# Performance work log

Measured on AMD Instinct MI355X. Metric: run time of the kernel, lower is better.

Reference implementation:

```python
import jax, jax.numpy as jnp
import numpy as np

DIM = 1024
HEADS = 16
HEAD_DIM = DIM // HEADS


def rotate_half(x):
    x1, x2 = jnp.split(x, 2, axis=-1)
    return jnp.concatenate((-x2, x1), axis=-1)


def rope_tables(T, D, dtype=jnp.float32):
    inv_freq = 1.0 / (10000.0 ** (jnp.arange(0, D, 2, dtype=jnp.float32) / D))
    t = jnp.arange(T, dtype=jnp.float32)
    freqs = jnp.einsum('i,j->ij', t, inv_freq)  # [T, D/2]
    emb = jnp.concatenate((freqs, freqs), axis=-1)  # [T, D]
    return emb.astype(dtype), jnp.cos(emb).astype(dtype), jnp.sin(emb).astype(dtype)


def setup_inputs() -> dict:
    key = jax.random.key(0)
    kx, kq, kk, kv, ko = jax.random.split(key, 5)
    B, T = 2, 4096
    scale = 1.0 / np.sqrt(DIM)
    x = jax.random.normal(kx, (B, T, DIM), dtype=jnp.float32)
    wq = jax.random.normal(kq, (DIM, DIM), dtype=jnp.float32) * scale
    wk = jax.random.normal(kk, (DIM, DIM), dtype=jnp.float32) * scale
    wv = jax.random.normal(kv, (DIM, DIM), dtype=jnp.float32) * scale
    wo = jax.random.normal(ko, (DIM, DIM), dtype=jnp.float32) * scale
    return {"x": x, "wq": wq, "wk": wk, "wv": wv, "wo": wo}


def reference(x, wq, wk, wv, wo):
    B, T, C = x.shape
    H, D = HEADS, HEAD_DIM
    # projections; nn.Linear applies x @ W^T
    q = (x @ wq.T).reshape(B, T, H, D).transpose(0, 2, 1, 3)  # [B,H,T,D]
    k = (x @ wk.T).reshape(B, T, H, D).transpose(0, 2, 1, 3)
    v = (x @ wv.T).reshape(B, T, H, D).transpose(0, 2, 1, 3)
    _, cos, sin = rope_tables(T, D, x.dtype)
    cos = cos[None, None]  # [1,1,T,D]
    sin = sin[None, None]
    q = q * cos + rotate_half(q) * sin
    k = k * cos + rotate_half(k) * sin
    scores = jnp.einsum('bhtd,bhsd->bhts', q, k) / jnp.sqrt(jnp.asarray(D, x.dtype))
    attn = jax.nn.softmax(scores, axis=-1)
    out = jnp.einsum('bhts,bhsd->bhtd', attn, v)
    out = out.transpose(0, 2, 1, 3).reshape(B, T, C)
    return out @ wo.T
```

## Files before the change

### kernel.cpp

```cpp
#include <hip/hip_runtime.h>
#include <hip/hip_bf16.h>
#include <math.h>


typedef __attribute__((ext_vector_type(8))) short short8;
typedef __attribute__((ext_vector_type(4))) short short4v;
typedef __attribute__((ext_vector_type(4))) float floatx4;

using bf16 = __hip_bfloat16;

static constexpr int T_ = 4096;
static constexpr int C_ = 1024;
static constexpr int M_ = 8192;
static constexpr float QSCALE = 0.125f * 1.44269504088896340736f;

#if __has_builtin(__builtin_amdgcn_mfma_f32_16x16x16bf16_1k)
#define USE_K16 1
#else
#define USE_K16 0
#endif

#if __has_builtin(__builtin_amdgcn_exp2f)
#define EXP2 __builtin_amdgcn_exp2f
#else
#define EXP2 exp2f
#endif

__device__ __forceinline__ floatx4 mfma16(short8 a, short8 b, floatx4 c) {
    return __builtin_amdgcn_mfma_f32_16x16x32_bf16(a, b, c, 0, 0, 0);
}
#if USE_K16
__device__ __forceinline__ floatx4 mfma_k16(short4v a, short4v b, floatx4 c) {
    return __builtin_amdgcn_mfma_f32_16x16x16bf16_1k(a, b, c, 0, 0, 0);
}
#endif

__device__ __forceinline__ short8 ld8(const bf16* p) {
    return *reinterpret_cast<const short8*>(p);
}
__device__ __forceinline__ short4v ld4(const bf16* p) {
    return *reinterpret_cast<const short4v*>(p);
}
__device__ __forceinline__ void st8(bf16* p, short8 v) {
    *reinterpret_cast<short8*>(p) = v;
}
__device__ __forceinline__ unsigned short f2bf(float x) {
    bf16 h = __float2bfloat16(x);
    return reinterpret_cast<unsigned short&>(h);
}

__device__ __forceinline__ int pack2bf(float a, float b, unsigned sel) {
    const unsigned ua = __float_as_uint(a) + 0x8000u;
    const unsigned ub = __float_as_uint(b) + 0x8000u;
    int r;
    asm("v_perm_b32 %0, %1, %2, %3" : "=v"(r) : "v"(ub), "v"(ua), "s"(sel));
    return r;
}
__device__ __forceinline__ short4v i2s4(int lo, int hi) {
    union { int2 i; short4v s; } u;
    u.i.x = lo; u.i.y = hi;
    return u.s;
}
__device__ __forceinline__ short8 i2s8(int a, int b, int c, int d) {
    union { int4 i; short8 s; } u;
    u.i.x = a; u.i.y = b; u.i.z = c; u.i.w = d;
    return u.s;
}

__device__ __forceinline__ void cp16(const bf16* g, bf16* l) {
    __builtin_amdgcn_global_load_lds(
        (const __attribute__((address_space(1))) void*)g,
        (__attribute__((address_space(3))) void*)l, 16, 0, 0);
}

__global__ __launch_bounds__(256)
void prep_kernel(const float* __restrict__ x,
                 const float* __restrict__ wq, const float* __restrict__ wk,
                 const float* __restrict__ wv, const float* __restrict__ wo,
                 bf16* __restrict__ xb, bf16* __restrict__ wqb,
                 float2* __restrict__ CS) {
    const int blk = blockIdx.x;
    if (blk < 6144) {
        const float* in;
        bf16* out;
        int i;
        if (blk < 4096) {
            i = blk * 256 + threadIdx.x;
            in = x; out = xb;
        } else {
            i = (blk - 4096) * 256 + threadIdx.x;
            const int seg = i >> 17;
            const int off = i & 131071;
            in = (seg == 0) ? wq : (seg == 1) ? wk : (seg == 2) ? wv : wo;
            out = wqb + (size_t)i * 8 - (size_t)off * 8;
            i = off;
        }
        const float4* p = reinterpret_cast<const float4*>(in) + (size_t)i * 2;
        const float4 a = p[0];
        const float4 b = p[1];
        short8 v;
        v[0] = (short)f2bf(a.x); v[1] = (short)f2bf(a.y);
        v[2] = (short)f2bf(a.z); v[3] = (short)f2bf(a.w);
        v[4] = (short)f2bf(b.x); v[5] = (short)f2bf(b.y);
        v[6] = (short)f2bf(b.z); v[7] = (short)f2bf(b.w);
        *(reinterpret_cast<short8*>(out) + i) = v;
    } else {
        const int i = (blk - 6144) * 256 + threadIdx.x;
        const int t = i >> 5;
        const int j = i & 31;
        const float inv_freq = expf(-(float)j * 0.28782313662425575f);
        float s, c;
        sincosf((float)t * inv_freq, &s, &c);
        CS[i] = make_float2(c, s);
    }
}

#define GEMM_PROLOGUE(Ab, Wb)                                                 \
    _Pragma("unroll")                                                         \
    for (int j = 0; j < 2; ++j) {                                             \
        const int row = srow + j * 64;                                        \
        cp16((Ab) + (size_t)row * C_ + scol, &Als[0][(j * 256 + tid) * 8]);   \
        cp16((Wb) + (size_t)row * C_ + scol, &Bls[0][(j * 256 + tid) * 8]);   \
    }                                                                         \
    _Pragma("unroll")                                                         \
    for (int j = 0; j < 2; ++j) {                                             \
        const int row = srow + j * 64;                                        \
        cp16((Ab) + (size_t)row * C_ + 32 + scol, &Als[1][(j * 256 + tid) * 8]); \
        cp16((Wb) + (size_t)row * C_ + 32 + scol, &Bls[1][(j * 256 + tid) * 8]); \
    }

#define KSTEP(Ab, Wb, KK, BUF, LB, DOISSUE, VMN)                              \
    do {                                                                      \
        asm volatile("s_waitcnt vmcnt(" VMN ")" ::: "memory");                \
        __builtin_amdgcn_sched_barrier(0);                                    \
        __builtin_amdgcn_s_barrier();                                         \
        __builtin_amdgcn_sched_barrier(0);                                    \
        if (DOISSUE) {                                                        \
            _Pragma("unroll")                                                 \
            for (int j = 0; j < 2; ++j) {                                     \
                const int row = srow + j * 64;                                \
                cp16((Ab) + (size_t)row * C_ + (KK) + 64 + scol,              \
                     &Als[LB][(j * 256 + tid) * 8]);                          \
                cp16((Wb) + (size_t)row * C_ + (KK) + 64 + scol,              \
                     &Bls[LB][(j * 256 + tid) * 8]);                          \
            }                                                                 \
        }                                                                     \
        short8 a[4], b[4];                                                    \
        _Pragma("unroll")                                                     \
        for (int i = 0; i < 4; ++i)                                           \
            a[i] = ld8(&Als[BUF][(wr + i * 16 + lr) * 32 + quad * 8]);        \
        _Pragma("unroll")                                                     \
        for (int j = 0; j < 4; ++j)                                           \
            b[j] = ld8(&Bls[BUF][(wc + j * 16 + lr) * 32 + quad * 8]);        \
        _Pragma("unroll")                                                     \
        for (int i = 0; i < 4; ++i)                                           \
            _Pragma("unroll")                                                 \
            for (int j = 0; j < 4; ++j)                                       \
                acc[i][j] = mfma16(a[i], b[j], acc[i][j]);                    \
    } while (0)

#define GEMM_MAINLOOP(Ab, Wb)                                                 \
    GEMM_PROLOGUE(Ab, Wb)                                                     \
    for (int kk = 0; kk < 960; kk += 96) {                                    \
        KSTEP(Ab, Wb, kk,      0, 2, 1, "4");                                 \
        KSTEP(Ab, Wb, kk + 32, 1, 0, 1, "4");                                 \
        KSTEP(Ab, Wb, kk + 64, 2, 1, 1, "4");                                 \
    }                                                                         \
    KSTEP(Ab, Wb, 960, 0, 2, 0, "4");                                         \
    KSTEP(Ab, Wb, 992, 1, 0, 0, "0");

__global__ __launch_bounds__(256)
void gemm128_kernel(const bf16* __restrict__ A, const bf16* __restrict__ W,
                    void* __restrict__ out, int mode, int ntile, int cpx) {
    const int orig = blockIdx.x;
    const int swz  = (orig & 7) * cpx + (orig >> 3);
    const int m0   = (swz / ntile) * 128;
    const int n0   = (swz % ntile) * 128;
    const int tid  = threadIdx.x;
    const int lane = tid & 63;
    const int wave = tid >> 6;
    const int quad = lane >> 4;
    const int lr   = lane & 15;
    const int wr   = (wave >> 1) * 64;
    const int wc   = (wave & 1) * 64;

    __shared__ __align__(16) bf16 Als[3][128 * 32];
    __shared__ __align__(16) bf16 Bls[3][128 * 32];

    const int srow = tid >> 2;
    const int scol = (tid & 3) * 8;

    floatx4 acc[4][4];
#pragma unroll
    for (int i = 0; i < 4; ++i)
#pragma unroll
        for (int j = 0; j < 4; ++j) acc[i][j] = floatx4{0.f, 0.f, 0.f, 0.f};

    const bf16* Ab = A + (size_t)m0 * C_;
    const bf16* Wb = W + (size_t)n0 * C_;

    GEMM_MAINLOOP(Ab, Wb)

    if (mode == 0) {
        bf16* ob = (bf16*)out;
#pragma unroll
        for (int j = 0; j < 4; ++j) {
            const int col = n0 + wc + j * 16 + lr;
#pragma unroll
            for (int i = 0; i < 4; ++i)
#pragma unroll
                for (int r = 0; r < 4; ++r) {
                    const int m = m0 + wr + i * 16 + quad * 4 + r;
                    ob[(size_t)m * C_ + col] = __float2bfloat16(acc[i][j][r]);
                }
        }
    } else {
        float* of = (float*)out;
#pragma unroll
        for (int j = 0; j < 4; ++j) {
            const int col = n0 + wc + j * 16 + lr;
#pragma unroll
            for (int i = 0; i < 4; ++i)
#pragma unroll
                for (int r = 0; r < 4; ++r) {
                    const int m = m0 + wr + i * 16 + quad * 4 + r;
                    of[(size_t)m * C_ + col] = acc[i][j][r];
                }
        }
    }
}

__global__ __launch_bounds__(256)
void gemm_qkv_kernel(const bf16* __restrict__ A, const bf16* __restrict__ W,
                     bf16* __restrict__ Qbase, const float2* __restrict__ CS) {
    const int orig = blockIdx.x;
    const int swz  = (orig & 7) * 192 + (orig >> 3);
    const int m0   = (swz / 24) * 128;
    const int n0g  = (swz % 24) * 128;
    const int tid  = threadIdx.x;
    const int lane = tid & 63;
    const int wave = tid >> 6;
    const int quad = lane >> 4;
    const int lr   = lane & 15;
    const int wr   = (wave >> 1) * 64;
    const int wc   = (wave & 1) * 64;

    __shared__ __align__(16) bf16 Als[3][128 * 32];
    __shared__ __align__(16) bf16 Bls[3][128 * 32];

    const int srow = tid >> 2;
    const int scol = (tid & 3) * 8;

    floatx4 acc[4][4];
#pragma unroll
    for (int i = 0; i < 4; ++i)
#pragma unroll
        for (int j = 0; j < 4; ++j) acc[i][j] = floatx4{0.f, 0.f, 0.f, 0.f};

    const bf16* Ab = A + (size_t)m0 * C_;
    const bf16* Wb = W + (size_t)n0g * C_;

    GEMM_MAINLOOP(Ab, Wb)

    const int seg = n0g >> 10;
    const int n0  = n0g & 1023;
    if (seg < 2) {
        bf16* ob = Qbase + (size_t)seg * M_ * C_;
        const float scale = (seg == 0) ? QSCALE : 1.0f;
        const int tb = (m0 & 4095) + wr + quad * 4;
#pragma unroll
        for (int j = 0; j < 2; ++j) {
            const int col  = n0 + wc + j * 16 + lr;
            const int jcol = j * 16 + lr;
#pragma unroll
            for (int i = 0; i < 4; ++i) {
#pragma unroll
                for (int r = 0; r < 4; ++r) {
                    const int t = tb + i * 16 + r;
                    const float2 cs = CS[t * 32 + jcol];
                    const float q1 = acc[i][j][r];
                    const float q2 = acc[i][j + 2][r];
                    const int m = m0 + wr + i * 16 + quad * 4 + r;
                    ob[(size_t)m * C_ + col] =
                        __float2bfloat16((q1 * cs.x - q2 * cs.y) * scale);
                    ob[(size_t)m * C_ + col + 32] =
                        __float2bfloat16((q2 * cs.x + q1 * cs.y) * scale);
                }
            }
        }
    } else {
        unsigned short* ob = (unsigned short*)(Qbase + (size_t)2 * M_ * C_);
        const int b2 = m0 >> 12;
#pragma unroll
        for (int j = 0; j < 4; ++j) {
            const int n = n0 + wc + j * 16 + lr;
            const int h = n >> 6;
            const int d = n & 63;
#pragma unroll
            for (int i = 0; i < 4; ++i) {
                const int t0 = (m0 & 4095) + wr + i * 16 + quad * 4;
                ushort4 v;
                v.x = f2bf(acc[i][j][0]); v.y = f2bf(acc[i][j][1]);
                v.z = f2bf(acc[i][j][2]); v.w = f2bf(acc[i][j][3]);
                size_t idx = ((size_t)((b2 * 16 + h) * 64 + d)) * T_ + t0;
                *reinterpret_cast<ushort4*>(ob + idx) = v;
            }
        }
    }
}

__global__ __launch_bounds__(256)
void attn_kernel(const bf16* __restrict__ Q, const bf16* __restrict__ K,
                 const bf16* __restrict__ Vt, bf16* __restrict__ AO) {
    const int tid  = threadIdx.x;
    const int lane = tid & 63;
    const int wave = tid >> 6;
    const int quad = lane >> 4;
    const int lr   = lane & 15;
    const int bh   = blockIdx.y;
    const int b    = bh >> 4;
    const int h    = bh & 15;
    const int q0   = blockIdx.x * 128 + wave * 32;

    const bf16* Qb = Q + (size_t)b * T_ * C_ + h * 64;
    const bf16* Kb = K + (size_t)b * T_ * C_ + h * 64;
    const bf16* Vb = Vt + (size_t)bh * 64 * T_;

#if USE_K16
    __shared__ __align__(16) bf16 Kls[2][64 * 64];
    __shared__ __align__(16) bf16 Vls[2][64 * 64];

    const int srow  = tid >> 3;
    const int sc    = tid & 7;
    const int sphys = (sc ^ (srow & 7)) * 8;
    const int soff0 = srow * 64 + sphys;
    const int soff1 = (srow + 32) * 64 + sphys;

    const unsigned psel = 0x07060302u;
    const floatx4 FZ = {0.f, 0.f, 0.f, 0.f};
    const int one2 = 0x3F803F80;
    const short8 VONE = i2s8(one2, one2, one2, one2);

    short8 aq[2][2];
#pragma unroll
    for (int t = 0; t < 2; ++t) {
        aq[t][0] = ld8(Qb + (size_t)(q0 + t * 16 + lr) * C_ + quad * 8);
        aq[t][1] = ld8(Qb + (size_t)(q0 + t * 16 + lr) * C_ + 32 + quad * 8);
    }

    floatx4 O[2][4];
#pragma unroll
    for (int t = 0; t < 2; ++t)
#pragma unroll
        for (int dt = 0; dt < 4; ++dt) O[t][dt] = floatx4{0.f, 0.f, 0.f, 0.f};
    floatx4 Osum[2] = {{0.f, 0.f, 0.f, 0.f}, {0.f, 0.f, 0.f, 0.f}};

    const int lr7    = lr & 7;
    const int kchunk = (quad ^ lr7) * 8;
    const int vsub   = (quad & 1) * 4;
    const int vbq    = quad >> 1;
    const int kel0   = lr * 64 + kchunk;
    const int kel1   = kel0 ^ 32;
    int velk[4];
#pragma unroll
    for (int kk = 0; kk < 4; ++kk)
        velk[kk] = lr * 64 + (((2 * kk + vbq) ^ lr7) * 8) + vsub;

    short8 kr0, kr1, vr0, vr1;
#define LOAD_STAGE(kv0)                                              \
    do {                                                             \
        kr0 = ld8(Kb + (size_t)((kv0) + srow) * C_ + sc * 8);        \
        kr1 = ld8(Kb + (size_t)((kv0) + srow + 32) * C_ + sc * 8);   \
        vr0 = ld8(Vb + (size_t)srow * T_ + (kv0) + sc * 8);          \
        vr1 = ld8(Vb + (size_t)(srow + 32) * T_ + (kv0) + sc * 8);   \
    } while (0)
#define STORE_STAGE(p)                                               \
    do {                                                             \
        st8(&Kls[p][soff0], kr0);                                    \
        st8(&Kls[p][soff1], kr1);                                    \
        st8(&Vls[p][soff0], vr0);                                    \
        st8(&Vls[p][soff1], vr1);                                    \
    } while (0)

#define BAR()                                                        \
    do {                                                             \
        asm volatile("s_waitcnt lgkmcnt(0)" ::: "memory");           \
        __builtin_amdgcn_s_barrier();                                \
    } while (0)

#define COMPUTE(P)                                                            \
    do {                                                                      \
        const bf16* Ks = Kls[P];                                              \
        const bf16* Vs = Vls[P];                                              \
        int prlo[2][4], prhi[2][4];                                           \
        _Pragma("unroll")                                                     \
        for (int kk = 0; kk < 4; ++kk) {                                      \
            const short8 kf0 = ld8(Ks + kk * 1024 + kel0);                    \
            const short8 kf1 = ld8(Ks + kk * 1024 + kel1);                    \
            floatx4 s0 = mfma16(kf0, aq[0][0], FZ);                           \
            s0 = mfma16(kf1, aq[0][1], s0);                                   \
            floatx4 s1 = mfma16(kf0, aq[1][0], FZ);                           \
            s1 = mfma16(kf1, aq[1][1], s1);                                   \
            const float e0 = EXP2(s0[0]), e1 = EXP2(s0[1]);                   \
            const float e2 = EXP2(s0[2]), e3 = EXP2(s0[3]);                   \
            prlo[0][kk] = pack2bf(e0, e1, psel);                              \
            prhi[0][kk] = pack2bf(e2, e3, psel);                              \
            const float f0 = EXP2(s1[0]), f1 = EXP2(s1[1]);                   \
            const float f2 = EXP2(s1[2]), f3 = EXP2(s1[3]);                   \
            prlo[1][kk] = pack2bf(f0, f1, psel);                              \
            prhi[1][kk] = pack2bf(f2, f3, psel);                              \
        }                                                                     \
        \
        Osum[0] = mfma16(i2s8(prlo[0][0], prhi[0][0], prlo[0][1], prhi[0][1]),\
                         VONE, Osum[0]);                                      \
        Osum[0] = mfma16(i2s8(prlo[0][2], prhi[0][2], prlo[0][3], prhi[0][3]),\
                         VONE, Osum[0]);                                      \
        Osum[1] = mfma16(i2s8(prlo[1][0], prhi[1][0], prlo[1][1], prhi[1][1]),\
                         VONE, Osum[1]);                                      \
        Osum[1] = mfma16(i2s8(prlo[1][2], prhi[1][2], prlo[1][3], prhi[1][3]),\
                         VONE, Osum[1]);                                      \
        __builtin_amdgcn_s_setprio(1);                                        \
        _Pragma("unroll")                                                     \
        for (int dt = 0; dt < 4; ++dt) {                                      \
            _Pragma("unroll")                                                 \
            for (int kk = 0; kk < 4; ++kk) {                                  \
                const short4v vf = ld4(Vs + dt * 1024 + velk[kk]);            \
                O[0][dt] = mfma_k16(i2s4(prlo[0][kk], prhi[0][kk]), vf, O[0][dt]); \
                O[1][dt] = mfma_k16(i2s4(prlo[1][kk], prhi[1][kk]), vf, O[1][dt]); \
            }                                                                 \
        }                                                                     \
        __builtin_amdgcn_s_setprio(0);                                        \
    } while (0)

    LOAD_STAGE(0);
    STORE_STAGE(0);
    LOAD_STAGE(64);
    BAR();

    constexpr int NS = T_ / 64;
    for (int s = 0; s < NS; s += 2) {
        if (s + 1 < NS) STORE_STAGE(1);
        if (s + 2 < NS) LOAD_STAGE((s + 2) * 64);
        COMPUTE(0);
        BAR();
        if (s + 2 < NS) STORE_STAGE(0);
        if (s + 3 < NS) LOAD_STAGE((s + 3) * 64);
        COMPUTE(1);
        BAR();
    }

#pragma unroll
    for (int t = 0; t < 2; ++t) {
#pragma unroll
        for (int r = 0; r < 4; ++r) {
            const float inv = 1.0f / fmaxf(Osum[t][r], 1e-30f);
            const size_t row =
                (size_t)(b * T_ + q0 + t * 16 + quad * 4 + r) * C_ + h * 64;
            AO[row + 0  + lr] = __float2bfloat16(O[t][0][r] * inv);
            AO[row + 16 + lr] = __float2bfloat16(O[t][1][r] * inv);
            AO[row + 32 + lr] = __float2bfloat16(O[t][2][r] * inv);
            AO[row + 48 + lr] = __float2bfloat16(O[t][3][r] * inv);
        }
    }
#undef LOAD_STAGE
#undef STORE_STAGE
#undef COMPUTE
#undef BAR
#else
    __shared__ __align__(16) unsigned short Pbuf[4][512];
    unsigned short* Pw = Pbuf[wave];
    for (int half = 0; half < 2; ++half) {
        const int qh = q0 + half * 16;
        const short8 aq0 = ld8(Qb + (size_t)(qh + lr) * C_ + quad * 8);
        const short8 aq1 = ld8(Qb + (size_t)(qh + lr) * C_ + 32 + quad * 8);
        floatx4 O0 = {0,0,0,0}, O1 = {0,0,0,0}, O2 = {0,0,0,0}, O3 = {0,0,0,0};
        float lrun[4] = {0.f, 0.f, 0.f, 0.f};
        for (int kv = 0; kv < T_; kv += 32) {
            floatx4 S0 = {0,0,0,0}, S1 = {0,0,0,0};
            const bf16* k0 = Kb + (size_t)(kv + lr) * C_ + quad * 8;
            const bf16* k1 = Kb + (size_t)(kv + 16 + lr) * C_ + quad * 8;
            S0 = mfma16(aq0, ld8(k0), S0);
            S0 = mfma16(aq1, ld8(k0 + 32), S0);
            S1 = mfma16(aq0, ld8(k1), S1);
            S1 = mfma16(aq1, ld8(k1 + 32), S1);
#pragma unroll
            for (int r = 0; r < 4; ++r) {
                const float e0 = exp2f(S0[r]);
                const float e1 = exp2f(S1[r]);
                lrun[r] += e0 + e1;
                const int row = quad * 4 + r;
                Pw[row * 32 + lr]      = f2bf(e0);
                Pw[row * 32 + 16 + lr] = f2bf(e1);
            }
            __syncthreads();
            const short8 ap = *reinterpret_cast<const short8*>(Pw + lr * 32 + quad * 8);
            O0 = mfma16(ap, ld8(Vb + (size_t)(lr)      * T_ + kv + quad * 8), O0);
            O1 = mfma16(ap, ld8(Vb + (size_t)(16 + lr) * T_ + kv + quad * 8), O1);
            O2 = mfma16(ap, ld8(Vb + (size_t)(32 + lr) * T_ + kv + quad * 8), O2);
            O3 = mfma16(ap, ld8(Vb + (size_t)(48 + lr) * T_ + kv + quad * 8), O3);
            __syncthreads();
        }
#pragma unroll
        for (int r = 0; r < 4; ++r) {
            float l = lrun[r];
            l += __shfl_xor(l, 1); l += __shfl_xor(l, 2);
            l += __shfl_xor(l, 4); l += __shfl_xor(l, 8);
            const float inv = 1.0f / fmaxf(l, 1e-30f);
            const size_t row = (size_t)(b * T_ + qh + quad * 4 + r) * C_ + h * 64;
            AO[row + 0  + lr] = __float2bfloat16(O0[r] * inv);
            AO[row + 16 + lr] = __float2bfloat16(O1[r] * inv);
            AO[row + 32 + lr] = __float2bfloat16(O2[r] * inv);
            AO[row + 48 + lr] = __float2bfloat16(O3[r] * inv);
        }
    }
#endif
}

extern "C" void kernel_launch(void* const* d_in, const int* in_sizes, int n_in,
                              void* d_out, int out_size, void* d_ws, size_t ws_size,
                              hipStream_t stream) {
    const float* x  = (const float*)d_in[0];
    const float* wq = (const float*)d_in[1];
    const float* wk = (const float*)d_in[2];
    const float* wv = (const float*)d_in[3];
    const float* wo = (const float*)d_in[4];
    float* out = (float*)d_out;

    bf16* xb  = (bf16*)d_ws;
    bf16* wqb = xb  + (size_t)M_ * C_;
    bf16* wkb = wqb + (size_t)C_ * C_;
    bf16* wvb = wkb + (size_t)C_ * C_;
    bf16* wob = wvb + (size_t)C_ * C_;
    bf16* Q   = wob + (size_t)C_ * C_;
    bf16* K   = Q   + (size_t)M_ * C_;
    bf16* Vt  = K   + (size_t)M_ * C_;
    float2* CS = (float2*)(Vt + (size_t)M_ * C_);
    bf16* AO  = xb;

    prep_kernel<<<6656, 256, 0, stream>>>(x, wq, wk, wv, wo, xb, wqb, CS);

    gemm_qkv_kernel<<<1536, 256, 0, stream>>>(xb, wqb, Q, CS);

    attn_kernel<<<dim3(T_ / 128, 32), 256, 0, stream>>>(Q, K, Vt, AO);

    gemm128_kernel<<<512, 256, 0, stream>>>(AO, wob, out, 2, 8, 64);
}
```

Measured before the change: 376.1 us.

## Widen GEMM tiles to 128x256 for QKV and output projections

Both GEMM kernels now compute 128x256 output tiles per block, with each wave holding a 64x128 accumulator tile, which doubles B-tile reuse of each A fragment from LDS. Grid sizes are halved and the swizzle parameters are adjusted to match, and the RoPE epilogue is remapped so that column pairs at offset 32 stay within one head. The aim is to cut global and LDS traffic per FLOP. In exchange, register pressure roughly doubles (128 accumulator floats per thread), LDS use grows, and the output GEMM launches only 256 blocks, which may underfill the GPU's compute units.

Measured after the change: 410.8 us. +9.2%, slower.

```diff
diff --git a/kernel.cpp b/kernel.cpp
--- a/kernel.cpp
+++ b/kernel.cpp
@@ -115,19 +115,17 @@
     }
 }
 
-#define GEMM_PROLOGUE(Ab, Wb)                                                 \
-    _Pragma("unroll")                                                         \
-    for (int j = 0; j < 2; ++j) {                                             \
-        const int row = srow + j * 64;                                        \
-        cp16((Ab) + (size_t)row * C_ + scol, &Als[0][(j * 256 + tid) * 8]);   \
-        cp16((Wb) + (size_t)row * C_ + scol, &Bls[0][(j * 256 + tid) * 8]);   \
-    }                                                                         \
-    _Pragma("unroll")                                                         \
-    for (int j = 0; j < 2; ++j) {                                             \
-        const int row = srow + j * 64;                                        \
-        cp16((Ab) + (size_t)row * C_ + 32 + scol, &Als[1][(j * 256 + tid) * 8]); \
-        cp16((Wb) + (size_t)row * C_ + 32 + scol, &Bls[1][(j * 256 + tid) * 8]); \
-    }
+#define GEMM_STAGE(Ab, Wb, KK, BUF)                                           \
+    do {                                                                      \
+        _Pragma("unroll")                                                     \
+        for (int j = 0; j < 2; ++j)                                           \
+            cp16((Ab) + (size_t)(srow + j * 64) * C_ + (KK) + scol,           \
+                 &Als[BUF][(j * 256 + tid) * 8]);                             \
+        _Pragma("unroll")                                                     \
+        for (int j = 0; j < 4; ++j)                                           \
+            cp16((Wb) + (size_t)(srow + j * 64) * C_ + (KK) + scol,           \
+                 &Bls[BUF][(j * 256 + tid) * 8]);                             \
+    } while (0)
 
 #define KSTEP(Ab, Wb, KK, BUF, LB, DOISSUE, VMN)                              \
     do {                                                                      \
@@ -135,38 +133,30 @@
         __builtin_amdgcn_sched_barrier(0);                                    \
         __builtin_amdgcn_s_barrier();                                         \
         __builtin_amdgcn_sched_barrier(0);                                    \
-        if (DOISSUE) {                                                        \
-            _Pragma("unroll")                                                 \
-            for (int j = 0; j < 2; ++j) {                                     \
-                const int row = srow + j * 64;                                \
-                cp16((Ab) + (size_t)row * C_ + (KK) + 64 + scol,              \
-                     &Als[LB][(j * 256 + tid) * 8]);                          \
-                cp16((Wb) + (size_t)row * C_ + (KK) + 64 + scol,              \
-                     &Bls[LB][(j * 256 + tid) * 8]);                          \
-            }                                                                 \
-        }                                                                     \
-        short8 a[4], b[4];                                                    \
+        if (DOISSUE) GEMM_STAGE(Ab, Wb, (KK) + 64, LB);                       \
+        short8 a[4], b[8];                                                    \
         _Pragma("unroll")                                                     \
         for (int i = 0; i < 4; ++i)                                           \
             a[i] = ld8(&Als[BUF][(wr + i * 16 + lr) * 32 + quad * 8]);        \
         _Pragma("unroll")                                                     \
-        for (int j = 0; j < 4; ++j)                                           \
+        for (int j = 0; j < 8; ++j)                                           \
             b[j] = ld8(&Bls[BUF][(wc + j * 16 + lr) * 32 + quad * 8]);        \
         _Pragma("unroll")                                                     \
         for (int i = 0; i < 4; ++i)                                           \
             _Pragma("unroll")                                                 \
-            for (int j = 0; j < 4; ++j)                                       \
+            for (int j = 0; j < 8; ++j)                                       \
                 acc[i][j] = mfma16(a[i], b[j], acc[i][j]);                    \
     } while (0)
 
 #define GEMM_MAINLOOP(Ab, Wb)                                                 \
-    GEMM_PROLOGUE(Ab, Wb)                                                     \
+    GEMM_STAGE(Ab, Wb, 0, 0);                                                 \
+    GEMM_STAGE(Ab, Wb, 32, 1);                                                \
     for (int kk = 0; kk < 960; kk += 96) {                                    \
-        KSTEP(Ab, Wb, kk,      0, 2, 1, "4");                                 \
-        KSTEP(Ab, Wb, kk + 32, 1, 0, 1, "4");                                 \
-        KSTEP(Ab, Wb, kk + 64, 2, 1, 1, "4");                                 \
+        KSTEP(Ab, Wb, kk,      0, 2, 1, "6");                                 \
+        KSTEP(Ab, Wb, kk + 32, 1, 0, 1, "6");                                 \
+        KSTEP(Ab, Wb, kk + 64, 2, 1, 1, "6");                                 \
     }                                                                         \
-    KSTEP(Ab, Wb, 960, 0, 2, 0, "4");                                         \
+    KSTEP(Ab, Wb, 960, 0, 2, 0, "6");                                         \
     KSTEP(Ab, Wb, 992, 1, 0, 0, "0");
 
 __global__ __launch_bounds__(256)
@@ -175,26 +165,26 @@
     const int orig = blockIdx.x;
     const int swz  = (orig & 7) * cpx + (orig >> 3);
     const int m0   = (swz / ntile) * 128;
-    const int n0   = (swz % ntile) * 128;
+    const int n0   = (swz % ntile) * 256;
     const int tid  = threadIdx.x;
     const int lane = tid & 63;
     const int wave = tid >> 6;
     const int quad = lane >> 4;
     const int lr   = lane & 15;
     const int wr   = (wave >> 1) * 64;
-    const int wc   = (wave & 1) * 64;
+    const int wc   = (wave & 1) * 128;
 
     __shared__ __align__(16) bf16 Als[3][128 * 32];
-    __shared__ __align__(16) bf16 Bls[3][128 * 32];
+    __shared__ __align__(16) bf16 Bls[3][256 * 32];
 
     const int srow = tid >> 2;
     const int scol = (tid & 3) * 8;
 
-    floatx4 acc[4][4];
+    floatx4 acc[4][8];
 #pragma unroll
     for (int i = 0; i < 4; ++i)
 #pragma unroll
-        for (int j = 0; j < 4; ++j) acc[i][j] = floatx4{0.f, 0.f, 0.f, 0.f};
+        for (int j = 0; j < 8; ++j) acc[i][j] = floatx4{0.f, 0.f, 0.f, 0.f};
 
     const bf16* Ab = A + (size_t)m0 * C_;
     const bf16* Wb = W + (size_t)n0 * C_;
@@ -204,7 +194,7 @@
     if (mode == 0) {
         bf16* ob = (bf16*)out;
 #pragma unroll
-        for (int j = 0; j < 4; ++j) {
+        for (int j = 0; j < 8; ++j) {
             const int col = n0 + wc + j * 16 + lr;
 #pragma unroll
             for (int i = 0; i < 4; ++i)
@@ -217,7 +207,7 @@
     } else {
         float* of = (float*)out;
 #pragma unroll
-        for (int j = 0; j < 4; ++j) {
+        for (int j = 0; j < 8; ++j) {
             const int col = n0 + wc + j * 16 + lr;
 #pragma unroll
             for (int i = 0; i < 4; ++i)
@@ -234,28 +224,28 @@
 void gemm_qkv_kernel(const bf16* __restrict__ A, const bf16* __restrict__ W,
                      bf16* __restrict__ Qbase, const float2* __restrict__ CS) {
     const int orig = blockIdx.x;
-    const int swz  = (orig & 7) * 192 + (orig >> 3);
-    const int m0   = (swz / 24) * 128;
-    const int n0g  = (swz % 24) * 128;
+    const int swz  = (orig & 7) * 96 + (orig >> 3);
+    const int m0   = (swz / 12) * 128;
+    const int n0g  = (swz % 12) * 256;
     const int tid  = threadIdx.x;
     const int lane = tid & 63;
     const int wave = tid >> 6;
     const int quad = lane >> 4;
     const int lr   = lane & 15;
     const int wr   = (wave >> 1) * 64;
-    const int wc   = (wave & 1) * 64;
+    const int wc   = (wave & 1) * 128;
 
     __shared__ __align__(16) bf16 Als[3][128 * 32];
-    __shared__ __align__(16) bf16 Bls[3][128 * 32];
+    __shared__ __align__(16) bf16 Bls[3][256 * 32];
 
     const int srow = tid >> 2;
     const int scol = (tid & 3) * 8;
 
-    floatx4 acc[4][4];
+    floatx4 acc[4][8];
 #pragma unroll
     for (int i = 0; i < 4; ++i)
 #pragma unroll
-        for (int j = 0; j < 4; ++j) acc[i][j] = floatx4{0.f, 0.f, 0.f, 0.f};
+        for (int j = 0; j < 8; ++j) acc[i][j] = floatx4{0.f, 0.f, 0.f, 0.f};
 
     const bf16* Ab = A + (size_t)m0 * C_;
     const bf16* Wb = W + (size_t)n0g * C_;
@@ -268,18 +258,20 @@
         bf16* ob = Qbase + (size_t)seg * M_ * C_;
         const float scale = (seg == 0) ? QSCALE : 1.0f;
         const int tb = (m0 & 4095) + wr + quad * 4;
-#pragma unroll
-        for (int j = 0; j < 2; ++j) {
-            const int col  = n0 + wc + j * 16 + lr;
-            const int jcol = j * 16 + lr;
+        const int jps[4] = {0, 1, 4, 5};
+#pragma unroll
+        for (int jj = 0; jj < 4; ++jj) {
+            const int jp   = jps[jj];
+            const int col  = n0 + wc + jp * 16 + lr;
+            const int jcol = (jp & 1) * 16 + lr;
 #pragma unroll
             for (int i = 0; i < 4; ++i) {
 #pragma unroll
                 for (int r = 0; r < 4; ++r) {
                     const int t = tb + i * 16 + r;
                     const float2 cs = CS[t * 32 + jcol];
-                    const float q1 = acc[i][j][r];
-                    const float q2 = acc[i][j + 2][r];
+                    const float q1 = acc[i][jp][r];
+                    const float q2 = acc[i][jp + 2][r];
                     const int m = m0 + wr + i * 16 + quad * 4 + r;
                     ob[(size_t)m * C_ + col] =
                         __float2bfloat16((q1 * cs.x - q2 * cs.y) * scale);
@@ -292,7 +284,7 @@
         unsigned short* ob = (unsigned short*)(Qbase + (size_t)2 * M_ * C_);
         const int b2 = m0 >> 12;
 #pragma unroll
-        for (int j = 0; j < 4; ++j) {
+        for (int j = 0; j < 8; ++j) {
             const int n = n0 + wc + j * 16 + lr;
             const int h = n >> 6;
             const int d = n & 63;
@@ -539,9 +531,9 @@
 
     prep_kernel<<<6656, 256, 0, stream>>>(x, wq, wk, wv, wo, xb, wqb, CS);
 
-    gemm_qkv_kernel<<<1536, 256, 0, stream>>>(xb, wqb, Q, CS);
+    gemm_qkv_kernel<<<768, 256, 0, stream>>>(xb, wqb, Q, CS);
 
     attn_kernel<<<dim3(T_ / 128, 32), 256, 0, stream>>>(Q, K, Vt, AO);
 
-    gemm128_kernel<<<512, 256, 0, stream>>>(AO, wob, out, 2, 8, 64);
-}
+    gemm128_kernel<<<256, 256, 0, stream>>>(AO, wob, out, 2, 4, 32);
+}
```
